# Optimization experiments

Hardware: AMD Instinct MI355X
Metric: run time of the kernel (lower is better)

## Reference

```python
import jax, jax.numpy as jnp
import numpy as np


def recursive_fht(x):
    # Faithful vectorized version of the module's recursive butterfly FHT
    # (twiddle = cas(2*pi*n/N), no flipped-odd term, exactly as in the source).
    N = x.shape[-1]
    if N == 1:
        return x
    e = recursive_fht(x[..., ::2])
    o = recursive_fht(x[..., 1::2])
    n = jnp.arange(N // 2, dtype=x.dtype)
    t = jnp.cos(2 * jnp.pi * n / N) + jnp.sin(2 * jnp.pi * n / N)
    return jnp.concatenate([e + t * o, e - t * o], axis=-1)


def compl_mul1d(x1, x2):
    # x1: [B, i, modes], x2: [i, o, modes]; flips along axis 0 as in the source
    x1f = x1[::-1]
    x2f = x2[::-1]
    return 0.5 * (jnp.einsum('bix,iox->box', x1, x2)
                  - jnp.einsum('bix,iox->box', x1f, x2f)
                  + jnp.einsum('bix,iox->box', x1, x2f)
                  + jnp.einsum('bix,iox->box', x1f, x2))


def idht(X):
    # Inverse discrete Hartley transform via the cas matrix (DHT is an
    # involution up to 1/K). K = N//2+1 is not a power of 2, so a dense
    # transform is used. Compute-bound batched GEMM.
    K = X.shape[-1]
    n = jnp.arange(K, dtype=X.dtype)
    ang = 2.0 * jnp.pi * jnp.outer(n, n) / K
    cas = jnp.cos(ang) + jnp.sin(ang)  # [K, K]
    return jnp.einsum('bck,kn->bcn', X, cas) / K


def setup_inputs() -> dict:
    key = jax.random.key(0)
    k1, k2 = jax.random.split(key)
    B, Cin, Cout, N, modes1 = 32, 64, 64, 4096, 1024
    x = jax.random.normal(k1, (B, Cin, N), dtype=jnp.float32)
    scale = 1.0 / (Cin * Cout)
    weights1 = scale * jax.random.uniform(k2, (Cin, Cout, modes1), dtype=jnp.float32)
    return {"x": x, "weights1": weights1, "modes1": modes1}


def reference(x, weights1, modes1):
    B, C, N = x.shape
    # dht with threshold=1.0: FHT along last axis, low-pass filter is a no-op
    x_ht = recursive_fht(x)
    K = N // 2 + 1
    out_ht = jnp.zeros((B, C, K), dtype=x.dtype)
    out_ht = out_ht.at[:, :, :modes1].set(compl_mul1d(x_ht[:, :, :modes1], weights1))
    return idht(out_ht)  # [B, C, N//2+1]
```

## Files before the change

kernel.cpp:

```cpp
#include <hip/hip_runtime.h>
#include <hip/hip_bf16.h>

#define BATCH 32
#define CIN   64
#define COUT  64
#define NFFT  4096
#define MODES 1024
#define KOUT  2049
#define NPAD  2176

typedef __bf16 bf16x8 __attribute__((ext_vector_type(8)));
typedef float  f32x4  __attribute__((ext_vector_type(4)));

#define AS1 __attribute__((address_space(1)))
#define AS3 __attribute__((address_space(3)))

static __device__ __forceinline__ void gl_lds16(const void* g, void* l) {
    __builtin_amdgcn_global_load_lds((const AS1 void*)g, (AS3 void*)l, 16, 0, 0);
}

static __device__ __forceinline__ void bfly4(float eA, float eB, float oA, float oB,
                                             float t, float c0, float c1,
                                             float& w0, float& w1, float& w2, float& w3) {
    float PA = fmaf(t, oA, eA), MA = fmaf(-t, oA, eA);
    float PB = fmaf(t, oB, eB), MB = fmaf(-t, oB, eB);
    w0 = fmaf(c0, PB, PA);
    w2 = fmaf(-c0, PB, PA);
    w1 = fmaf(c1, MB, MA);
    w3 = fmaf(-c1, MB, MA);
}


__global__ void fill_tw(float* __restrict__ tw) {
    int t = blockIdx.x * blockDim.x + threadIdx.x;
    if (t >= NFFT) return;
    if (t == 0) { tw[0] = 1.0f; return; }
    int h = 1 << (31 - __clz(t));
    int n = t - h;
    float ang = 3.14159265358979323846f * (float)n / (float)h;
    tw[t] = cosf(ang) + sinf(ang);
}

__global__ void fill_c2t(__hip_bfloat16* __restrict__ hi) {
    int idx = blockIdx.x * blockDim.x + threadIdx.x;
    if (idx >= NPAD * MODES) return;
    int n = idx >> 10;
    int k = idx & 1023;
    float v = 0.0f;
    if (n < KOUT) {
        int m = (k * n) % KOUT;
        float ang = 6.28318530717958647692f * (float)m / (float)KOUT;
        v = (cosf(ang) + sinf(ang)) * (1.0f / (float)KOUT);
    }
    hi[idx] = __float2bfloat16(v);
}

__global__ __launch_bounds__(256) void fht_kernel(const float* __restrict__ x,
                                                  const float* __restrict__ tw,
                                                  float* __restrict__ xh) {
    __shared__ __align__(16) float bufA[NFFT];
    __shared__ __align__(16) float bufB[NFFT];
    const int tid = threadIdx.x;
    const int row = blockIdx.x;
    const float4* xr = (const float4*)(x + (size_t)row * NFFT);
    float4* bA4 = (float4*)bufA;
#pragma unroll
    for (int j = 0; j < 4; ++j) bA4[tid + j * 256] = xr[tid + j * 256];
    __syncthreads();

    float* src = bufA;
    float* dst = bufB;

    {
#pragma unroll
        for (int q = 0; q < 4; ++q) {
            const int u = tid + q * 256;
            float eA = src[u];
            float eB = src[u + 1024];
            float oA = src[u + 2048];
            float oB = src[u + 3072];
            float PA = eA + oA, MA = eA - oA;
            float PB = eB + oB, MB = eB - oB;
            dst[u]        = PA + PB;
            dst[u + 2048] = PA - PB;
            dst[u + 1024] = MA + MB;
            dst[u + 3072] = MA - MB;
        }
        __syncthreads();
        float* tmp = src; src = dst; dst = tmp;
    }

#pragma unroll
    for (int p = 1; p < 3; ++p) {
        const int s = 2 * p;
        const int L = 1 << s;
        const int shift = 11 - s;
        const int hq = 1 << (shift - 1);
#pragma unroll
        for (int q = 0; q < 4; ++q) {
            const int u = tid + q * 256;
            const int kap = __builtin_amdgcn_readfirstlane(u >> (shift - 1));
            const int gp = u & (hq - 1);
            const int b0 = (kap << (shift + 1)) + gp;
            float eA = src[b0];
            float eB = src[b0 + hq];
            float oA = src[b0 + 2 * hq];
            float oB = src[b0 + 3 * hq];
            float t  = tw[L + kap], c0 = tw[2 * L + kap], c1 = tw[3 * L + kap];
            float w0, w1, w2, w3;
            bfly4(eA, eB, oA, oB, t, c0, c1, w0, w1, w2, w3);
            dst[u]        = w0;
            dst[u + 1024] = w1;
            dst[u + 2048] = w2;
            dst[u + 3072] = w3;
        }
        __syncthreads();
        float* tmp = src; src = dst; dst = tmp;
    }

#pragma unroll
    for (int p = 3; p < 5; ++p) {
        const int s = 2 * p;
        const int L = 1 << s;
        const int shift = 11 - s;
        const int hq = 1 << (shift - 1);
        const int u0 = 4 * tid;
        const int kap = u0 >> (shift - 1);
        const int gp = u0 & (hq - 1);
        const int b0 = (kap << (shift + 1)) + gp;
        float4 V0 = *(const float4*)(src + b0);
        float4 V1 = *(const float4*)(src + b0 + hq);
        float4 V2 = *(const float4*)(src + b0 + 2 * hq);
        float4 V3 = *(const float4*)(src + b0 + 3 * hq);
        float t  = tw[L + kap], c0 = tw[2 * L + kap], c1 = tw[3 * L + kap];
        float4 W0, W1, W2, W3;
        bfly4(V0.x, V1.x, V2.x, V3.x, t, c0, c1, W0.x, W1.x, W2.x, W3.x);
        bfly4(V0.y, V1.y, V2.y, V3.y, t, c0, c1, W0.y, W1.y, W2.y, W3.y);
        bfly4(V0.z, V1.z, V2.z, V3.z, t, c0, c1, W0.z, W1.z, W2.z, W3.z);
        bfly4(V0.w, V1.w, V2.w, V3.w, t, c0, c1, W0.w, W1.w, W2.w, W3.w);
        *(float4*)(dst + u0)        = W0;
        *(float4*)(dst + u0 + 1024) = W1;
        *(float4*)(dst + u0 + 2048) = W2;
        *(float4*)(dst + u0 + 3072) = W3;
        __syncthreads();
        float* tmp = src; src = dst; dst = tmp;
    }

    {
        const int u0 = 4 * tid;
        float4 R0 = *(const float4*)(src + 4 * u0);
        float4 R1 = *(const float4*)(src + 4 * u0 + 4);
        float4 R2 = *(const float4*)(src + 4 * u0 + 8);
        float4 R3 = *(const float4*)(src + 4 * u0 + 12);
        float4 T  = *(const float4*)(tw + 1024 + u0);
        float4 C0 = *(const float4*)(tw + 2048 + u0);
        float4 C1 = *(const float4*)(tw + 3072 + u0);
        float4 W0, W1, W2, W3;
        bfly4(R0.x, R0.y, R0.z, R0.w, T.x, C0.x, C1.x, W0.x, W1.x, W2.x, W3.x);
        bfly4(R1.x, R1.y, R1.z, R1.w, T.y, C0.y, C1.y, W0.y, W1.y, W2.y, W3.y);
        bfly4(R2.x, R2.y, R2.z, R2.w, T.z, C0.z, C1.z, W0.z, W1.z, W2.z, W3.z);
        bfly4(R3.x, R3.y, R3.z, R3.w, T.w, C0.w, C1.w, W0.w, W1.w, W2.w, W3.w);
        *(float4*)(dst + u0)        = W0;
        *(float4*)(dst + u0 + 1024) = W1;
        *(float4*)(dst + u0 + 2048) = W2;
        *(float4*)(dst + u0 + 3072) = W3;
        __syncthreads();
        float* tmp = src; src = dst; dst = tmp;
    }

    ((float4*)(xh + (size_t)row * MODES))[tid] = ((const float4*)src)[tid];
}

__global__ __launch_bounds__(256) void mix_kernel(const f32x4* __restrict__ xh,
                                                  const f32x4* __restrict__ w,
                                                  ushort4* __restrict__ y_hi) {
    const int kl = threadIdx.x & 63;
    const int jg = threadIdx.x >> 6;
    const int k4 = blockIdx.x * 64 + kl;
    const int b  = blockIdx.y;
    const int rb = (BATCH - 1) - b;
    const int o  = blockIdx.z * 4 + jg;

    f32x4 accb = (f32x4){0.f, 0.f, 0.f, 0.f};
    f32x4 accr = (f32x4){0.f, 0.f, 0.f, 0.f};

#pragma unroll 4
    for (int i = 0; i < 32; ++i) {
        const int mi = 63 - i;
        f32x4 xai = xh[(size_t)(b  * CIN + i ) * 256 + k4];
        f32x4 xam = xh[(size_t)(b  * CIN + mi) * 256 + k4];
        f32x4 xbi = xh[(size_t)(rb * CIN + i ) * 256 + k4];
        f32x4 xbm = xh[(size_t)(rb * CIN + mi) * 256 + k4];
        f32x4 w1 = w[(size_t)(i  * COUT + o) * 256 + k4];
        f32x4 w2 = w[(size_t)(mi * COUT + o) * 256 + k4];
        f32x4 sa = xai + xam;
        f32x4 da = xai - xam;
        f32x4 sb = xbi + xbm;
        f32x4 db = xbi - xbm;
        f32x4 wp = w1 + w2, wm = w1 - w2;
        accb += sa * wp + db * wm;
        accr += sb * wp + da * wm;
    }

    const size_t ib = (size_t)(b  * COUT + o) * 256 + k4;
    const size_t ir = (size_t)(rb * COUT + o) * 256 + k4;
    f32x4 vb = accb * 0.5f;
    f32x4 vr = accr * 0.5f;
    __hip_bfloat16 b0 = __float2bfloat16(vb.x), b1 = __float2bfloat16(vb.y),
                   b2 = __float2bfloat16(vb.z), b3 = __float2bfloat16(vb.w);
    __hip_bfloat16 r0 = __float2bfloat16(vr.x), r1 = __float2bfloat16(vr.y),
                   r2 = __float2bfloat16(vr.z), r3 = __float2bfloat16(vr.w);
    y_hi[ib] = make_ushort4(*(unsigned short*)&b0, *(unsigned short*)&b1,
                            *(unsigned short*)&b2, *(unsigned short*)&b3);
    y_hi[ir] = make_ushort4(*(unsigned short*)&r0, *(unsigned short*)&r1,
                            *(unsigned short*)&r2, *(unsigned short*)&r3);
}

__global__ __launch_bounds__(256) void idht_mfma(const __hip_bfloat16* __restrict__ yh,
                                                 const __hip_bfloat16* __restrict__ ch,
                                                 float* __restrict__ out) {
    __shared__ __align__(16) char sa[2][16 * 1024];
    __shared__ __align__(16) char sb[2][8 * 1024];

    const int tid  = threadIdx.x;
    const int lane = tid & 63;
    const int wave = tid >> 6;
    const int wm = wave & 1;
    const int wn = wave >> 1;
    const int rbase = blockIdx.x * 128;
    const int nbase = blockIdx.y * 64;

    const int lrow = (lane & 15) * 2048;
    const int lchk = (lane >> 4) * 16;

    const char* ga  = (const char*)yh + (size_t)rbase * 2048;
    const char* gbh = (const char*)ch + (size_t)nbase * 2048;

    f32x4 acc[4][2];
#pragma unroll
    for (int mt = 0; mt < 4; ++mt)
#pragma unroll
        for (int nt = 0; nt < 2; ++nt) acc[mt][nt] = (f32x4){0.f, 0.f, 0.f, 0.f};

    auto stage = [&](int bi, int k0) {
#pragma unroll
        for (int r = 0; r < 4; ++r) {
            int ab = wave + r * 4;
            gl_lds16(ga + (size_t)(ab >> 1) * 32768 + lrow + (ab & 1) * 64 + lchk + k0 * 2,
                     sa[bi] + ab * 1024);
        }
#pragma unroll
        for (int r = 0; r < 2; ++r) {
            int bb = wave + r * 4;
            gl_lds16(gbh + (size_t)(bb >> 1) * 32768 + lrow + (bb & 1) * 64 + lchk + k0 * 2,
                     sb[bi] + bb * 1024);
        }
    };

    stage(0, 0);
    int cur = 0;
    for (int ks = 0; ks < MODES / 64; ++ks) {
        __syncthreads();
        if (ks + 1 < MODES / 64) stage(1 - cur, (ks + 1) * 64);
#pragma unroll
        for (int kc = 0; kc < 2; ++kc) {
            bf16x8 a_[4], b_[2];
#pragma unroll
            for (int mt = 0; mt < 4; ++mt)
                a_[mt] = *(const bf16x8*)(sa[cur] + ((wm * 4 + mt) * 2 + kc) * 1024 + lane * 16);
#pragma unroll
            for (int nt = 0; nt < 2; ++nt)
                b_[nt] = *(const bf16x8*)(sb[cur] + ((wn * 2 + nt) * 2 + kc) * 1024 + lane * 16);
#pragma unroll
            for (int mt = 0; mt < 4; ++mt)
#pragma unroll
                for (int nt = 0; nt < 2; ++nt)
                    acc[mt][nt] = __builtin_amdgcn_mfma_f32_16x16x32_bf16(a_[mt], b_[nt], acc[mt][nt], 0, 0, 0);
        }
        cur ^= 1;
    }

#pragma unroll
    for (int mt = 0; mt < 4; ++mt) {
        int row = rbase + wm * 64 + mt * 16 + (lane >> 4) * 4;
#pragma unroll
        for (int nt = 0; nt < 2; ++nt) {
            int col = nbase + wn * 32 + nt * 16 + (lane & 15);
            if (col < KOUT) {
#pragma unroll
                for (int r = 0; r < 4; ++r)
                    out[(size_t)(row + r) * KOUT + col] = acc[mt][nt][r];
            }
        }
    }
}

extern "C" void kernel_launch(void* const* d_in, const int* in_sizes, int n_in,
                              void* d_out, int out_size, void* d_ws, size_t ws_size,
                              hipStream_t stream) {
    const float* x = (const float*)d_in[0];
    const float* w = (const float*)d_in[1];
    float* out = (float*)d_out;

    float* tw = (float*)d_ws;
    float* xh = tw + NFFT;
    __hip_bfloat16* y_hi = (__hip_bfloat16*)(xh + (size_t)BATCH * CIN * MODES);
    __hip_bfloat16* c2h  = y_hi + (size_t)BATCH * COUT * MODES;

    fill_tw<<<NFFT / 256, 256, 0, stream>>>(tw);
    fill_c2t<<<(NPAD * MODES + 255) / 256, 256, 0, stream>>>(c2h);
    fht_kernel<<<BATCH * CIN, 256, 0, stream>>>(x, tw, xh);
    mix_kernel<<<dim3(4, 16, 16), 256, 0, stream>>>((const f32x4*)xh, (const f32x4*)w,
                                                    (ushort4*)y_hi);
    idht_mfma<<<dim3((BATCH * COUT) / 128, NPAD / 64), 256, 0, stream>>>(y_hi, c2h, out);
}
```

Before: 164.6 us.

## Register-resident radix-16 FHT stages and halve idht K-step staging

The FHT kernel is restructured so that pairs of radix-4 stages run in registers, leaving two padded LDS exchanges instead of six ping-pong passes with a barrier after each. The final stage writes only the needed first 1024 outputs straight from registers. Separately, the idht GEMM's K tile drops from 64 to 32, halving LDS buffers while doubling loop iterations and barriers. The FHT change cuts LDS traffic and syncs. The GEMM change may lose overlap per iteration but could raise occupancy.

```diff
diff --git a/kernel.cpp b/kernel.cpp
--- a/kernel.cpp
+++ b/kernel.cpp
@@ -58,117 +58,104 @@
 __global__ __launch_bounds__(256) void fht_kernel(const float* __restrict__ x,
                                                   const float* __restrict__ tw,
                                                   float* __restrict__ xh) {
-    __shared__ __align__(16) float bufA[NFFT];
-    __shared__ __align__(16) float bufB[NFFT];
-    const int tid = threadIdx.x;
+    __shared__ float ldsA[4352];
+    __shared__ float ldsB[4352];
+    const int t = threadIdx.x;
     const int row = blockIdx.x;
-    const float4* xr = (const float4*)(x + (size_t)row * NFFT);
-    float4* bA4 = (float4*)bufA;
-#pragma unroll
-    for (int j = 0; j < 4; ++j) bA4[tid + j * 256] = xr[tid + j * 256];
+    const float* xr = x + (size_t)row * NFFT;
+
+    float r[4][4];
+#pragma unroll
+    for (int a = 0; a < 4; ++a)
+#pragma unroll
+        for (int c = 0; c < 4; ++c)
+            r[a][c] = xr[t + 256 * a + 1024 * c];
+
+    float o1[4][4];
+#pragma unroll
+    for (int a = 0; a < 4; ++a) {
+        float PA = r[a][0] + r[a][2], MA = r[a][0] - r[a][2];
+        float PB = r[a][1] + r[a][3], MB = r[a][1] - r[a][3];
+        o1[a][0] = PA + PB;
+        o1[a][2] = PA - PB;
+        o1[a][1] = MA + MB;
+        o1[a][3] = MA - MB;
+    }
+    float o2[4][4];
+#pragma unroll
+    for (int kap = 0; kap < 4; ++kap) {
+        float tt = tw[4 + kap], c0 = tw[8 + kap], c1 = tw[12 + kap];
+        bfly4(o1[0][kap], o1[1][kap], o1[2][kap], o1[3][kap], tt, c0, c1,
+              o2[kap][0], o2[kap][1], o2[kap][2], o2[kap][3]);
+    }
+#pragma unroll
+    for (int kap = 0; kap < 4; ++kap)
+#pragma unroll
+        for (int c = 0; c < 4; ++c) {
+            int p = t + 256 * kap + 1024 * c;
+            ldsA[p + (p >> 4)] = o2[kap][c];
+        }
     __syncthreads();
 
-    float* src = bufA;
-    float* dst = bufB;
-
+    const int kap2 = t >> 4, gp = t & 15;
+    float r2[4][4];
+#pragma unroll
+    for (int a = 0; a < 4; ++a)
+#pragma unroll
+        for (int c = 0; c < 4; ++c) {
+            int p = 256 * kap2 + gp + 16 * a + 64 * c;
+            r2[a][c] = ldsA[p + (p >> 4)];
+        }
+    float o3[4][4];
     {
-#pragma unroll
-        for (int q = 0; q < 4; ++q) {
-            const int u = tid + q * 256;
-            float eA = src[u];
-            float eB = src[u + 1024];
-            float oA = src[u + 2048];
-            float oB = src[u + 3072];
-            float PA = eA + oA, MA = eA - oA;
-            float PB = eB + oB, MB = eB - oB;
-            dst[u]        = PA + PB;
-            dst[u + 2048] = PA - PB;
-            dst[u + 1024] = MA + MB;
-            dst[u + 3072] = MA - MB;
-        }
-        __syncthreads();
-        float* tmp = src; src = dst; dst = tmp;
-    }
-
-#pragma unroll
-    for (int p = 1; p < 3; ++p) {
-        const int s = 2 * p;
-        const int L = 1 << s;
-        const int shift = 11 - s;
-        const int hq = 1 << (shift - 1);
-#pragma unroll
-        for (int q = 0; q < 4; ++q) {
-            const int u = tid + q * 256;
-            const int kap = __builtin_amdgcn_readfirstlane(u >> (shift - 1));
-            const int gp = u & (hq - 1);
-            const int b0 = (kap << (shift + 1)) + gp;
-            float eA = src[b0];
-            float eB = src[b0 + hq];
-            float oA = src[b0 + 2 * hq];
-            float oB = src[b0 + 3 * hq];
-            float t  = tw[L + kap], c0 = tw[2 * L + kap], c1 = tw[3 * L + kap];
-            float w0, w1, w2, w3;
-            bfly4(eA, eB, oA, oB, t, c0, c1, w0, w1, w2, w3);
-            dst[u]        = w0;
-            dst[u + 1024] = w1;
-            dst[u + 2048] = w2;
-            dst[u + 3072] = w3;
-        }
-        __syncthreads();
-        float* tmp = src; src = dst; dst = tmp;
-    }
-
-#pragma unroll
-    for (int p = 3; p < 5; ++p) {
-        const int s = 2 * p;
-        const int L = 1 << s;
-        const int shift = 11 - s;
-        const int hq = 1 << (shift - 1);
-        const int u0 = 4 * tid;
-        const int kap = u0 >> (shift - 1);
-        const int gp = u0 & (hq - 1);
-        const int b0 = (kap << (shift + 1)) + gp;
-        float4 V0 = *(const float4*)(src + b0);
-        float4 V1 = *(const float4*)(src + b0 + hq);
-        float4 V2 = *(const float4*)(src + b0 + 2 * hq);
-        float4 V3 = *(const float4*)(src + b0 + 3 * hq);
-        float t  = tw[L + kap], c0 = tw[2 * L + kap], c1 = tw[3 * L + kap];
-        float4 W0, W1, W2, W3;
-        bfly4(V0.x, V1.x, V2.x, V3.x, t, c0, c1, W0.x, W1.x, W2.x, W3.x);
-        bfly4(V0.y, V1.y, V2.y, V3.y, t, c0, c1, W0.y, W1.y, W2.y, W3.y);
-        bfly4(V0.z, V1.z, V2.z, V3.z, t, c0, c1, W0.z, W1.z, W2.z, W3.z);
-        bfly4(V0.w, V1.w, V2.w, V3.w, t, c0, c1, W0.w, W1.w, W2.w, W3.w);
-        *(float4*)(dst + u0)        = W0;
-        *(float4*)(dst + u0 + 1024) = W1;
-        *(float4*)(dst + u0 + 2048) = W2;
-        *(float4*)(dst + u0 + 3072) = W3;
-        __syncthreads();
-        float* tmp = src; src = dst; dst = tmp;
-    }
-
+        float tt = tw[16 + kap2], c0 = tw[32 + kap2], c1 = tw[48 + kap2];
+#pragma unroll
+        for (int a = 0; a < 4; ++a)
+            bfly4(r2[a][0], r2[a][1], r2[a][2], r2[a][3], tt, c0, c1,
+                  o3[a][0], o3[a][1], o3[a][2], o3[a][3]);
+    }
+    float o4[4][4];
+#pragma unroll
+    for (int c = 0; c < 4; ++c) {
+        int kap3 = kap2 + 16 * c;
+        float tt = tw[64 + kap3], c0 = tw[128 + kap3], c1 = tw[192 + kap3];
+        bfly4(o3[0][c], o3[1][c], o3[2][c], o3[3][c], tt, c0, c1,
+              o4[c][0], o4[c][1], o4[c][2], o4[c][3]);
+    }
+#pragma unroll
+    for (int c = 0; c < 4; ++c)
+#pragma unroll
+        for (int cc = 0; cc < 4; ++cc) {
+            int p = t + 256 * c + 1024 * cc;
+            ldsB[p + (p >> 4)] = o4[c][cc];
+        }
+    __syncthreads();
+
+    float r3[4][4];
+#pragma unroll
+    for (int g = 0; g < 4; ++g)
+#pragma unroll
+        for (int c = 0; c < 4; ++c) {
+            int p = 16 * t + g + 4 * c;
+            r3[g][c] = ldsB[p + (p >> 4)];
+        }
+    float o5[4][4];
     {
-        const int u0 = 4 * tid;
-        float4 R0 = *(const float4*)(src + 4 * u0);
-        float4 R1 = *(const float4*)(src + 4 * u0 + 4);
-        float4 R2 = *(const float4*)(src + 4 * u0 + 8);
-        float4 R3 = *(const float4*)(src + 4 * u0 + 12);
-        float4 T  = *(const float4*)(tw + 1024 + u0);
-        float4 C0 = *(const float4*)(tw + 2048 + u0);
-        float4 C1 = *(const float4*)(tw + 3072 + u0);
-        float4 W0, W1, W2, W3;
-        bfly4(R0.x, R0.y, R0.z, R0.w, T.x, C0.x, C1.x, W0.x, W1.x, W2.x, W3.x);
-        bfly4(R1.x, R1.y, R1.z, R1.w, T.y, C0.y, C1.y, W0.y, W1.y, W2.y, W3.y);
-        bfly4(R2.x, R2.y, R2.z, R2.w, T.z, C0.z, C1.z, W0.z, W1.z, W2.z, W3.z);
-        bfly4(R3.x, R3.y, R3.z, R3.w, T.w, C0.w, C1.w, W0.w, W1.w, W2.w, W3.w);
-        *(float4*)(dst + u0)        = W0;
-        *(float4*)(dst + u0 + 1024) = W1;
-        *(float4*)(dst + u0 + 2048) = W2;
-        *(float4*)(dst + u0 + 3072) = W3;
-        __syncthreads();
-        float* tmp = src; src = dst; dst = tmp;
-    }
-
-    ((float4*)(xh + (size_t)row * MODES))[tid] = ((const float4*)src)[tid];
+        float tt = tw[256 + t], c0 = tw[512 + t], c1 = tw[768 + t];
+#pragma unroll
+        for (int g = 0; g < 4; ++g)
+            bfly4(r3[g][0], r3[g][1], r3[g][2], r3[g][3], tt, c0, c1,
+                  o5[g][0], o5[g][1], o5[g][2], o5[g][3]);
+    }
+    float* xo = xh + (size_t)row * MODES;
+#pragma unroll
+    for (int c = 0; c < 4; ++c) {
+        float tt = tw[1024 + t + 256 * c];
+        float c0 = tw[2048 + t + 256 * c];
+        float PA = fmaf(tt, o5[2][c], o5[0][c]);
+        float PB = fmaf(tt, o5[3][c], o5[1][c]);
+        xo[t + 256 * c] = fmaf(c0, PB, PA);
+    }
 }
 
 __global__ __launch_bounds__(256) void mix_kernel(const f32x4* __restrict__ xh,
@@ -219,8 +206,8 @@
 __global__ __launch_bounds__(256) void idht_mfma(const __hip_bfloat16* __restrict__ yh,
                                                  const __hip_bfloat16* __restrict__ ch,
                                                  float* __restrict__ out) {
-    __shared__ __align__(16) char sa[2][16 * 1024];
-    __shared__ __align__(16) char sb[2][8 * 1024];
+    __shared__ __align__(16) char sa[2][8 * 1024];
+    __shared__ __align__(16) char sb[2][4 * 1024];
 
     const int tid  = threadIdx.x;
     const int lane = tid & 63;
@@ -244,39 +231,32 @@
 
     auto stage = [&](int bi, int k0) {
 #pragma unroll
-        for (int r = 0; r < 4; ++r) {
-            int ab = wave + r * 4;
-            gl_lds16(ga + (size_t)(ab >> 1) * 32768 + lrow + (ab & 1) * 64 + lchk + k0 * 2,
-                     sa[bi] + ab * 1024);
-        }
-#pragma unroll
         for (int r = 0; r < 2; ++r) {
-            int bb = wave + r * 4;
-            gl_lds16(gbh + (size_t)(bb >> 1) * 32768 + lrow + (bb & 1) * 64 + lchk + k0 * 2,
-                     sb[bi] + bb * 1024);
-        }
+            int g = wave + r * 4;
+            gl_lds16(ga + (size_t)(g * 16) * 2048 + lrow + lchk + k0 * 2,
+                     sa[bi] + g * 1024);
+        }
+        gl_lds16(gbh + (size_t)(wave * 16) * 2048 + lrow + lchk + k0 * 2,
+                 sb[bi] + wave * 1024);
     };
 
     stage(0, 0);
     int cur = 0;
-    for (int ks = 0; ks < MODES / 64; ++ks) {
+    for (int ks = 0; ks < MODES / 32; ++ks) {
         __syncthreads();
-        if (ks + 1 < MODES / 64) stage(1 - cur, (ks + 1) * 64);
-#pragma unroll
-        for (int kc = 0; kc < 2; ++kc) {
-            bf16x8 a_[4], b_[2];
-#pragma unroll
-            for (int mt = 0; mt < 4; ++mt)
-                a_[mt] = *(const bf16x8*)(sa[cur] + ((wm * 4 + mt) * 2 + kc) * 1024 + lane * 16);
+        if (ks + 1 < MODES / 32) stage(cur ^ 1, (ks + 1) * 32);
+        bf16x8 a_[4], b_[2];
+#pragma unroll
+        for (int mt = 0; mt < 4; ++mt)
+            a_[mt] = *(const bf16x8*)(sa[cur] + (wm * 4 + mt) * 1024 + lane * 16);
+#pragma unroll
+        for (int nt = 0; nt < 2; ++nt)
+            b_[nt] = *(const bf16x8*)(sb[cur] + (wn * 2 + nt) * 1024 + lane * 16);
+#pragma unroll
+        for (int mt = 0; mt < 4; ++mt)
 #pragma unroll
             for (int nt = 0; nt < 2; ++nt)
-                b_[nt] = *(const bf16x8*)(sb[cur] + ((wn * 2 + nt) * 2 + kc) * 1024 + lane * 16);
-#pragma unroll
-            for (int mt = 0; mt < 4; ++mt)
-#pragma unroll
-                for (int nt = 0; nt < 2; ++nt)
-                    acc[mt][nt] = __builtin_amdgcn_mfma_f32_16x16x32_bf16(a_[mt], b_[nt], acc[mt][nt], 0, 0, 0);
-        }
+                acc[mt][nt] = __builtin_amdgcn_mfma_f32_16x16x32_bf16(a_[mt], b_[nt], acc[mt][nt], 0, 0, 0);
         cur ^= 1;
     }
 
```

New measurement: 161.0 us. -2.2%, faster.
